# Performance work log

Measured on AMD Instinct MI355X. Metric: run time of the kernel, lower is better.

## Reference

```python
import jax, jax.numpy as jnp
import numpy as np
from jax import lax

T, B, S = 64, 32, 64
V, E, H = 32000, 512, 512

def _p(key, shape, scale=0.05):
    return (jax.random.normal(key, shape, dtype=jnp.float32) * scale)

def setup_inputs() -> dict:
    key = jax.random.key(0)
    ks = jax.random.split(key, 24)
    inp = {
        'trg': jax.random.randint(ks[0], (T, B), 0, V),
        'encoded_src': jax.random.normal(ks[1], (S, B, 2 * H), dtype=jnp.float32),
        'emb': _p(ks[2], (V, E)),
        # LSTM layer 0: input = E + 2H
        'W_ih0': _p(ks[3], (4 * H, E + 2 * H)), 'W_hh0': _p(ks[4], (4 * H, H)),
        'b_ih0': _p(ks[5], (4 * H,)), 'b_hh0': _p(ks[6], (4 * H,)),
        # LSTM layer 1: input = H
        'W_ih1': _p(ks[7], (4 * H, H)), 'W_hh1': _p(ks[8], (4 * H, H)),
        'b_ih1': _p(ks[9], (4 * H,)), 'b_hh1': _p(ks[10], (4 * H,)),
        # attn_annot: 2H -> H
        'Wa': _p(ks[11], (H, 2 * H)), 'ba': _p(ks[12], (H,)),
        # attn_hidden: H -> H
        'Wh': _p(ks[13], (H, H)), 'bh': _p(ks[14], (H,)),
        # other: H -> 1
        'Wo': _p(ks[15], (1, H)), 'bo': _p(ks[16], (1,)),
        # penult: 3H -> E
        'Wp': _p(ks[17], (E, 3 * H)), 'bp': _p(ks[18], (E,)),
        # out bias (weight tied to emb)
        'b_out': _p(ks[19], (V,)),
    }
    return inp

def _lstm_cell(x, h, c, W_ih, W_hh, b_ih, b_hh):
    # PyTorch gate order: i, f, g, o
    g = x @ W_ih.T + b_ih + h @ W_hh.T + b_hh
    i, f, gg, o = jnp.split(g, 4, axis=-1)
    c_new = jax.nn.sigmoid(f) * c + jax.nn.sigmoid(i) * jnp.tanh(gg)
    h_new = jax.nn.sigmoid(o) * jnp.tanh(c_new)
    return h_new, c_new

def reference(trg, encoded_src, emb, W_ih0, W_hh0, b_ih0, b_hh0,
              W_ih1, W_hh1, b_ih1, b_hh1, Wa, ba, Wh, bh, Wo, bo,
              Wp, bp, b_out):
    trg_emb = emb[trg]                                # [T,B,E]
    annot_scores = encoded_src @ Wa.T + ba            # [S,B,H]
    Hd = W_hh0.shape[1]
    Bd = encoded_src.shape[1]
    h0 = jnp.zeros((2, Bd, Hd), dtype=encoded_src.dtype)
    c0 = jnp.zeros((2, Bd, Hd), dtype=encoded_src.dtype)
    ctx0 = jnp.zeros((Bd, encoded_src.shape[2]), dtype=encoded_src.dtype)

    def step(carry, emb_t):
        h, c, ctx = carry
        x = jnp.concatenate([emb_t, ctx], axis=1)      # [B, E+2H]
        h0n, c0n = _lstm_cell(x,   h[0], c[0], W_ih0, W_hh0, b_ih0, b_hh0)
        h1n, c1n = _lstm_cell(h0n, h[1], c[1], W_ih1, W_hh1, b_ih1, b_hh1)
        out = h1n                                      # [B,H]
        hs = out @ Wh.T + bh                           # [B,H]
        e = jnp.tanh(hs[None] + annot_scores) @ Wo.T + bo   # [S,B,1]
        a = jax.nn.softmax(e, axis=0)[..., 0]          # [S,B]
        ctx_new = jnp.einsum('sb,sbd->bd', a, encoded_src)  # [B,2H]
        stacked = jnp.concatenate([out, ctx_new], axis=1)   # [B,3H]
        return (jnp.stack([h0n, h1n]), jnp.stack([c0n, c1n]), ctx_new), stacked

    (h, c, _), all_scores = lax.scan(step, (h0, c0, ctx0), trg_emb)  # all_scores [T,B,3H]
    pen = all_scores @ Wp.T + bp                       # [T,B,E]
    logits = pen @ emb.T + b_out                       # [T,B,V] (tied weights)
    scores = jax.nn.log_softmax(logits, axis=2)
    return (scores, h, c)
```

## Files before the change

### kernel.cpp

```cpp
#include <hip/hip_runtime.h>


typedef unsigned short u16;
typedef short bf16x8 __attribute__((ext_vector_type(8)));
typedef float f32x4 __attribute__((ext_vector_type(4)));

#define MFMA_BF16(a, b, c) __builtin_amdgcn_mfma_f32_16x16x32_bf16((a), (b), (c), 0, 0, 0)

struct __attribute__((aligned(8))) U16x4 { u16 x, y, z, w; };

__device__ __forceinline__ float b2f(u16 u) {
  unsigned v = ((unsigned)u) << 16; float f; __builtin_memcpy(&f, &v, 4); return f;
}
__device__ __forceinline__ u16 f2b(float f) {
  unsigned u; __builtin_memcpy(&u, &f, 4);
  u = (u + 0x7FFFu + ((u >> 16) & 1u)) >> 16;
  return (u16)u;
}
__device__ __forceinline__ float sigm(float x) { return 1.f / (1.f + __expf(-x)); }
__device__ __forceinline__ float tanh_fast(float x) {
  x = fminf(fmaxf(x, -15.f), 15.f);
  float e = __expf(2.f * x);
  return (e - 1.f) / (e + 1.f);
}

__device__ __forceinline__ bf16x8 bl16(const u16* p) {
  bf16x8 v;
  asm volatile("global_load_dwordx4 %0, %1, off sc0 sc1" : "=v"(v) : "v"(p) : "memory");
  return v;
}
__device__ __forceinline__ float blf(const float* p) {
  float v;
  asm volatile("global_load_dword %0, %1, off sc0 sc1" : "=v"(v) : "v"(p) : "memory");
  return v;
}
__device__ __forceinline__ u16 blu16(const u16* p) {
  unsigned v;
  asm volatile("global_load_ushort %0, %1, off sc0 sc1" : "=v"(v) : "v"(p) : "memory");
  return (u16)v;
}
__device__ __forceinline__ void bs16(u16* p, u16 d) {
  unsigned dd = d;
  asm volatile("global_store_short %0, %1, off sc0 sc1" :: "v"(p), "v"(dd) : "memory");
}
__device__ __forceinline__ void bs32u(u16* p, unsigned d) {
  asm volatile("global_store_dword %0, %1, off sc0 sc1" :: "v"(p), "v"(d) : "memory");
}
__device__ __forceinline__ void bsf32(float* p, float d) {
  asm volatile("global_store_dword %0, %1, off sc0 sc1" :: "v"(p), "v"(d) : "memory");
}
__device__ __forceinline__ bf16x8 cl16(const u16* p) {
  bf16x8 v;
  asm volatile("global_load_dwordx4 %0, %1, off" : "=v"(v) : "v"(p));
  return v;
}
__device__ __forceinline__ void vmwait() {
  asm volatile("s_waitcnt vmcnt(0)" ::: "memory");
  __builtin_amdgcn_sched_barrier(0);
}

__global__ void f2b4_kernel(const float* __restrict__ src, u16* __restrict__ dst, long n4) {
  long i = (long)blockIdx.x * blockDim.x + threadIdx.x;
  long stride = (long)gridDim.x * blockDim.x;
  for (; i < n4; i += stride) {
    float4 v = ((const float4*)src)[i];
    U16x4 o; o.x = f2b(v.x); o.y = f2b(v.y); o.z = f2b(v.z); o.w = f2b(v.w);
    ((U16x4*)dst)[i] = o;
  }
}

__global__ void f2b4_strided(const float* __restrict__ src, u16* __restrict__ dst,
                             int rows, int cols4, int sld, int soff, int dld, int doff) {
  int total = rows * cols4;
  for (int i = blockIdx.x * blockDim.x + threadIdx.x; i < total; i += gridDim.x * blockDim.x) {
    int r = i / cols4, c4 = i - r * cols4;
    float4 v = *(const float4*)(src + (size_t)r * sld + soff + c4 * 4);
    U16x4 o; o.x = f2b(v.x); o.y = f2b(v.y); o.z = f2b(v.z); o.w = f2b(v.w);
    *(U16x4*)(dst + (size_t)r * dld + doff + c4 * 4) = o;
  }
}

__global__ void gather_emb_kernel(const int* __restrict__ trg, const float* __restrict__ emb,
                                  u16* __restrict__ out) {
  int r = blockIdx.x;
  int v = trg[r];
  const float* srow = emb + (size_t)v * 512;
  u16* drow = out + (size_t)r * 512;
  for (int e = threadIdx.x; e < 128; e += blockDim.x) {
    float4 x = ((const float4*)srow)[e];
    U16x4 o; o.x = f2b(x.x); o.y = f2b(x.y); o.z = f2b(x.z); o.w = f2b(x.w);
    ((U16x4*)drow)[e] = o;
  }
}

__global__ void annot_tr_kernel(const float* __restrict__ annot, u16* __restrict__ abt) {
  int b = blockIdx.x >> 6, s = blockIdx.x & 63;
  const float* src = annot + (size_t)(s * 32 + b) * 512;
  u16* dst = abt + (size_t)(b * 64 + s) * 512;
  int j = threadIdx.x;
  float4 v = ((const float4*)src)[j];
  U16x4 o; o.x = f2b(v.x); o.y = f2b(v.y); o.z = f2b(v.z); o.w = f2b(v.w);
  ((U16x4*)dst)[j] = o;
}

__global__ void enc_tr_kernel(const float* __restrict__ enc, u16* __restrict__ ebt) {
  int b = blockIdx.x >> 6, s = blockIdx.x & 63;
  const float* src = enc + (size_t)(s * 32 + b) * 1024;
  u16* dst = ebt + (size_t)(b * 64 + s) * 1024;
  int j = threadIdx.x;
  float4 v = ((const float4*)src)[j];
  U16x4 o; o.x = f2b(v.x); o.y = f2b(v.y); o.z = f2b(v.z); o.w = f2b(v.w);
  ((U16x4*)dst)[j] = o;
}

template <int MODE>
__global__ __launch_bounds__(256) void gemm_bt(
    const u16* __restrict__ A, const u16* __restrict__ B,
    float* __restrict__ outF, u16* __restrict__ outB,
    const float* __restrict__ bias0, const float* __restrict__ bias1,
    int N, int K) {
  const int l = threadIdx.x & 63, wv = threadIdx.x >> 6;
  const int m0 = blockIdx.x * 128 + wv * 32;
  const int n0 = blockIdx.y * 64;
  const int kg = ((l >> 4) << 3);
  const u16* Ap0 = A + (size_t)(m0 + (l & 15)) * K + kg;
  const u16* Ap1 = Ap0 + (size_t)16 * K;
  const u16* Bp = B + (size_t)(n0 + (l & 15)) * K + kg;
  f32x4 acc[2][4] = {};
  for (int k0 = 0; k0 < K; k0 += 32) {
    bf16x8 a0 = *(const bf16x8*)(Ap0 + k0);
    bf16x8 a1 = *(const bf16x8*)(Ap1 + k0);
#pragma unroll
    for (int nf = 0; nf < 4; ++nf) {
      bf16x8 bb = *(const bf16x8*)(Bp + (size_t)(nf * 16) * K + k0);
      acc[0][nf] = MFMA_BF16(a0, bb, acc[0][nf]);
      acc[1][nf] = MFMA_BF16(a1, bb, acc[1][nf]);
    }
  }
  float biasv[4];
#pragma unroll
  for (int nf = 0; nf < 4; ++nf) {
    int col = n0 + nf * 16 + (l & 15);
    float bv = bias0 ? bias0[col] : 0.f;
    if (bias1) bv += bias1[col];
    biasv[nf] = bv;
  }
#pragma unroll
  for (int mi = 0; mi < 2; ++mi)
#pragma unroll
    for (int i = 0; i < 4; ++i) {
      int row = m0 + mi * 16 + ((l >> 4) << 2) + i;
#pragma unroll
      for (int nf = 0; nf < 4; ++nf) {
        int col = n0 + nf * 16 + (l & 15);
        float v = acc[mi][nf][i] + biasv[nf];
        if constexpr (MODE == 1)
          outB[(size_t)row * N + col] = f2b(v);
        else
          outF[(size_t)row * N + col] = v;
      }
    }
}

__global__ __launch_bounds__(256) void logits_kernel(
    const u16* __restrict__ A,
    const u16* __restrict__ B,
    const float* __restrict__ bias,
    float* __restrict__ out,
    float* __restrict__ pmax, float* __restrict__ psum) {
  __shared__ float smf[128 * 132];
  const int id = blockIdx.x;
  const int lin = (id & 7) * 500 + (id >> 3);
  const int mt = lin & 15, nt = lin >> 4;
  const int gm = mt * 128, n0 = nt * 128;
  const int l = threadIdx.x & 63, wv = threadIdx.x >> 6;
  const int kg = ((l >> 4) << 3);
  const int m0 = gm + wv * 32;

  const u16* Ap0 = A + (size_t)(m0 + (l & 15)) * 512 + kg;
  const u16* Ap1 = Ap0 + (size_t)16 * 512;
  const u16* Bp = B + (size_t)(n0 + (l & 15)) * 512 + kg;
  f32x4 acc[2][8] = {};
  for (int k0 = 0; k0 < 512; k0 += 32) {
    bf16x8 a0 = *(const bf16x8*)(Ap0 + k0);
    bf16x8 a1 = *(const bf16x8*)(Ap1 + k0);
#pragma unroll
    for (int nf = 0; nf < 8; ++nf) {
      bf16x8 bb = *(const bf16x8*)(Bp + (size_t)(nf * 16) * 512 + k0);
      acc[0][nf] = MFMA_BF16(a0, bb, acc[0][nf]);
      acc[1][nf] = MFMA_BF16(a1, bb, acc[1][nf]);
    }
  }
  float bv[8];
#pragma unroll
  for (int nf = 0; nf < 8; ++nf) bv[nf] = bias[n0 + nf * 16 + (l & 15)];

  float lm[2][4], se[2][4];
#pragma unroll
  for (int mi = 0; mi < 2; ++mi)
#pragma unroll
    for (int i = 0; i < 4; ++i) {
      int rl = wv * 32 + mi * 16 + ((l >> 4) << 2) + i;
      float m_ = -3.4e38f;
#pragma unroll
      for (int nf = 0; nf < 8; ++nf) {
        float v = acc[mi][nf][i] + bv[nf];
        acc[mi][nf][i] = v;
        smf[rl * 132 + nf * 16 + (l & 15)] = v;
        m_ = fmaxf(m_, v);
      }
      lm[mi][i] = m_;
    }
#pragma unroll
  for (int d = 1; d < 16; d <<= 1)
#pragma unroll
    for (int mi = 0; mi < 2; ++mi)
#pragma unroll
      for (int i = 0; i < 4; ++i) lm[mi][i] = fmaxf(lm[mi][i], __shfl_xor(lm[mi][i], d));
#pragma unroll
  for (int mi = 0; mi < 2; ++mi)
#pragma unroll
    for (int i = 0; i < 4; ++i) {
      float s_ = 0.f;
#pragma unroll
      for (int nf = 0; nf < 8; ++nf) s_ += __expf(acc[mi][nf][i] - lm[mi][i]);
      se[mi][i] = s_;
    }
#pragma unroll
  for (int d = 1; d < 16; d <<= 1)
#pragma unroll
    for (int mi = 0; mi < 2; ++mi)
#pragma unroll
      for (int i = 0; i < 4; ++i) se[mi][i] += __shfl_xor(se[mi][i], d);
  if ((l & 15) == 0) {
#pragma unroll
    for (int mi = 0; mi < 2; ++mi)
#pragma unroll
      for (int i = 0; i < 4; ++i) {
        int row = m0 + mi * 16 + ((l >> 4) << 2) + i;
        pmax[(size_t)row * 250 + nt] = lm[mi][i];
        psum[(size_t)row * 250 + nt] = se[mi][i];
      }
  }
  __syncthreads();
#pragma unroll
  for (int r = 0; r < 128; r += 8) {
    int row = r + (threadIdx.x >> 5);
    int c4 = threadIdx.x & 31;
    float4 v = *(float4*)&smf[row * 132 + c4 * 4];
    *(float4*)&out[(size_t)(gm + row) * 32000 + n0 + c4 * 4] = v;
  }
}

__device__ __forceinline__ void grid_barrier(unsigned* flags, unsigned phase) {
  __syncthreads();
  if (threadIdx.x == 0) {
    __hip_atomic_store(flags + blockIdx.x * 32, phase, __ATOMIC_RELAXED,
                       __HIP_MEMORY_SCOPE_AGENT);
  }
  if (threadIdx.x < 32) {
    int spins = 0;
    while (__hip_atomic_load(flags + threadIdx.x * 32, __ATOMIC_RELAXED,
                             __HIP_MEMORY_SCOPE_AGENT) < phase &&
           spins < 2000000) ++spins;
  }
  __syncthreads();
}

__global__ __launch_bounds__(512, 2) void scan_kernel(
    const u16* __restrict__ xW0,
    const u16* __restrict__ Wcat0,
    const u16* __restrict__ Wcat1,
    const u16* __restrict__ Whb,
    const float* __restrict__ b_ih1, const float* __restrict__ b_hh1,
    const float* __restrict__ bh, const float* __restrict__ Wo, const float* __restrict__ bo,
    const u16* __restrict__ annot_bt,
    const u16* __restrict__ enc_bt,
    u16* __restrict__ ctxb,
    u16* __restrict__ h0b,
    u16* __restrict__ h1b,
    float* __restrict__ c0, float* __restrict__ c1,
    float* __restrict__ hs,
    u16* __restrict__ scoresb,
    float* __restrict__ dout_hc,
    unsigned* __restrict__ flags) {
  __shared__ float sm[16384];
  const int w = blockIdx.x;
  const int tid = threadIdx.x;
  const int l = tid & 63, wv = tid >> 6;
  const int jh0 = w * 16;
  const int bE = tid >> 4, jlE = tid & 15;
  unsigned phase = 0;

  float gb1[4];
#pragma unroll
  for (int g = 0; g < 4; ++g) gb1[g] = b_ih1[g * 512 + jh0 + jlE] + b_hh1[g * 512 + jh0 + jlE];
  const float bhv = bh[jh0 + jlE];
  const float bov = bo[0];

  for (int t = 0; t < 64; ++t) {
    const int pA = t & 1;
    {
      const int kg = ((l >> 4) << 3);
      u16 xw[4];
      {
        const u16* xp = xW0 + (size_t)(t * 32 + bE) * 2048 + jh0 + jlE;
#pragma unroll
        for (int g = 0; g < 4; ++g) xw[g] = blu16(xp + g * 512);
      }
      bf16x8 a0[6], a1[6];
#pragma unroll
      for (int kk = 0; kk < 6; ++kk) {
        const int k0 = wv * 192 + kk * 32;
        const u16* ab; int ld, off;
        if (k0 < 1024) { ab = ctxb; ld = 1024; off = k0; }
        else { ab = h0b + pA * 16384; ld = 512; off = k0 - 1024; }
        a0[kk] = bl16(ab + (size_t)(l & 15) * ld + off + kg);
        a1[kk] = bl16(ab + (size_t)((l & 15) + 16) * ld + off + kg);
      }
      vmwait();
      f32x4 acc[2][4] = {};
#pragma unroll
      for (int kk = 0; kk < 6; ++kk) {
        const int k0 = wv * 192 + kk * 32;
#pragma unroll
        for (int g = 0; g < 4; ++g) {
          bf16x8 bb = *(const bf16x8*)(Wcat0 + (size_t)(g * 512 + jh0 + (l & 15)) * 1536 + k0 + kg);
          acc[0][g] = MFMA_BF16(a0[kk], bb, acc[0][g]);
          acc[1][g] = MFMA_BF16(a1[kk], bb, acc[1][g]);
        }
      }
#pragma unroll
      for (int mi = 0; mi < 2; ++mi)
#pragma unroll
        for (int g = 0; g < 4; ++g)
#pragma unroll
          for (int i = 0; i < 4; ++i) {
            int m = mi * 16 + ((l >> 4) << 2) + i;
            sm[(wv * 32 + m) * 64 + g * 16 + (l & 15)] = acc[mi][g][i];
          }
      __syncthreads();
      {
        const int b = bE, jl = jlE, jh = jh0 + jl;
        float gate[4];
#pragma unroll
        for (int g = 0; g < 4; ++g) {
          float s = 0.f;
#pragma unroll
          for (int kv = 0; kv < 8; ++kv) s += sm[(kv * 32 + b) * 64 + g * 16 + jl];
          gate[g] = s + b2f(xw[g]);
        }
        float cn = sigm(gate[1]) * c0[b * 512 + jh] + sigm(gate[0]) * tanh_fast(gate[2]);
        float hn = sigm(gate[3]) * tanh_fast(cn);
        c0[b * 512 + jh] = cn;
        bs16(h0b + (pA ^ 1) * 16384 + b * 512 + jh, f2b(hn));
        if (t == 63) { dout_hc[b * 512 + jh] = hn; dout_hc[32768 + b * 512 + jh] = cn; }
      }
    }
    bf16x8 wB[16];
    {
      ++phase;
      __syncthreads();
      if (tid == 0)
        __hip_atomic_store(flags + blockIdx.x * 32, phase, __ATOMIC_RELAXED,
                           __HIP_MEMORY_SCOPE_AGENT);
      const int kg = ((l >> 4) << 3);
#pragma unroll
      for (int kk = 0; kk < 4; ++kk)
#pragma unroll
        for (int g = 0; g < 4; ++g)
          wB[kk * 4 + g] = cl16(Wcat1 + (size_t)(g * 512 + jh0 + (l & 15)) * 1024 +
                                wv * 128 + kk * 32 + kg);
      if (tid < 32) {
        int spins = 0;
        while (__hip_atomic_load(flags + tid * 32, __ATOMIC_RELAXED,
                                 __HIP_MEMORY_SCOPE_AGENT) < phase &&
               spins < 2000000) ++spins;
      }
      __syncthreads();
    }
    {
      const int kg = ((l >> 4) << 3);
      bf16x8 a0[4], a1[4];
#pragma unroll
      for (int kk = 0; kk < 4; ++kk) {
        const int k0 = wv * 128 + kk * 32;
        const u16* ab; int off;
        if (k0 < 512) { ab = h0b + (pA ^ 1) * 16384; off = k0; }
        else { ab = h1b + pA * 16384; off = k0 - 512; }
        a0[kk] = bl16(ab + (size_t)(l & 15) * 512 + off + kg);
        a1[kk] = bl16(ab + (size_t)((l & 15) + 16) * 512 + off + kg);
      }
      vmwait();
      f32x4 acc[2][4] = {};
#pragma unroll
      for (int kk = 0; kk < 4; ++kk) {
#pragma unroll
        for (int g = 0; g < 4; ++g) {
          acc[0][g] = MFMA_BF16(a0[kk], wB[kk * 4 + g], acc[0][g]);
          acc[1][g] = MFMA_BF16(a1[kk], wB[kk * 4 + g], acc[1][g]);
        }
      }
#pragma unroll
      for (int mi = 0; mi < 2; ++mi)
#pragma unroll
        for (int g = 0; g < 4; ++g)
#pragma unroll
          for (int i = 0; i < 4; ++i) {
            int m = mi * 16 + ((l >> 4) << 2) + i;
            sm[(wv * 32 + m) * 64 + g * 16 + (l & 15)] = acc[mi][g][i];
          }
      __syncthreads();
      {
        const int b = bE, jl = jlE, jh = jh0 + jl;
        float gate[4];
#pragma unroll
        for (int g = 0; g < 4; ++g) {
          float s = 0.f;
#pragma unroll
          for (int kv = 0; kv < 8; ++kv) s += sm[(kv * 32 + b) * 64 + g * 16 + jl];
          gate[g] = s + gb1[g];
        }
        float cn = sigm(gate[1]) * c1[b * 512 + jh] + sigm(gate[0]) * tanh_fast(gate[2]);
        float hn = sigm(gate[3]) * tanh_fast(cn);
        c1[b * 512 + jh] = cn;
        u16 hb = f2b(hn);
        bs16(h1b + (pA ^ 1) * 16384 + b * 512 + jh, hb);
        bs16(scoresb + (size_t)(t * 32 + b) * 1536 + jh, hb);
        if (t == 63) { dout_hc[16384 + b * 512 + jh] = hn; dout_hc[49152 + b * 512 + jh] = cn; }
      }
    }
    bf16x8 wC[2];
    {
      ++phase;
      __syncthreads();
      if (tid == 0)
        __hip_atomic_store(flags + blockIdx.x * 32, phase, __ATOMIC_RELAXED,
                           __HIP_MEMORY_SCOPE_AGENT);
      const int kg = ((l >> 4) << 3);
#pragma unroll
      for (int kk = 0; kk < 2; ++kk)
        wC[kk] = cl16(Whb + (size_t)(jh0 + (l & 15)) * 512 + wv * 64 + kk * 32 + kg);
      if (tid < 32) {
        int spins = 0;
        while (__hip_atomic_load(flags + tid * 32, __ATOMIC_RELAXED,
                                 __HIP_MEMORY_SCOPE_AGENT) < phase &&
               spins < 2000000) ++spins;
      }
      __syncthreads();
    }
    {
      const int kg = ((l >> 4) << 3);
      const u16* h1n = h1b + (pA ^ 1) * 16384;
      bf16x8 a0[2], a1[2];
#pragma unroll
      for (int kk = 0; kk < 2; ++kk) {
        const int k0 = wv * 64 + kk * 32;
        a0[kk] = bl16(h1n + (size_t)(l & 15) * 512 + k0 + kg);
        a1[kk] = bl16(h1n + (size_t)((l & 15) + 16) * 512 + k0 + kg);
      }
      vmwait();
      f32x4 acc2[2] = {};
#pragma unroll
      for (int kk = 0; kk < 2; ++kk) {
        acc2[0] = MFMA_BF16(a0[kk], wC[kk], acc2[0]);
        acc2[1] = MFMA_BF16(a1[kk], wC[kk], acc2[1]);
      }
#pragma unroll
      for (int mi = 0; mi < 2; ++mi)
#pragma unroll
        for (int i = 0; i < 4; ++i)
          sm[(wv * 32 + mi * 16 + ((l >> 4) << 2) + i) * 16 + (l & 15)] = acc2[mi][i];
      __syncthreads();
      {
        const int b = bE, jl = jlE;
        float s = 0.f;
#pragma unroll
        for (int kv = 0; kv < 8; ++kv) s += sm[(kv * 32 + b) * 16 + jl];
        bsf32(hs + b * 512 + jh0 + jl, s + bhv);
      }
    }
    grid_barrier(flags, ++phase);
    {
      const int b = w;
      float* hs_s = sm;
      float* wo_s = sm + 512;
      float* red = sm + 1024;
      float* a_s = sm + 1536;
      float hv = blf(hs + b * 512 + tid);
      float wov = Wo[tid];
      vmwait();
      hs_s[tid] = hv;
      wo_s[tid] = wov;
      __syncthreads();
      const int s_ = tid >> 3, ks = tid & 7;
      const u16* arow = annot_bt + (size_t)(b * 64 + s_) * 512 + ks * 64;
      float accv = 0.f;
#pragma unroll
      for (int kk8 = 0; kk8 < 8; ++kk8) {
        bf16x8 av = *(const bf16x8*)(arow + kk8 * 8);
#pragma unroll
        for (int j = 0; j < 8; ++j) {
          int k = ks * 64 + kk8 * 8 + j;
          accv += tanh_fast(hs_s[k] + b2f((u16)av[j])) * wo_s[k];
        }
      }
      red[tid] = accv;
      __syncthreads();
      if (tid < 64) {
        float e = bov;
#pragma unroll
        for (int j = 0; j < 8; ++j) e += red[tid * 8 + j];
        float mx = e;
#pragma unroll
        for (int d = 1; d < 64; d <<= 1) mx = fmaxf(mx, __shfl_xor(mx, d));
        float p = __expf(e - mx);
        float ss = p;
#pragma unroll
        for (int d = 1; d < 64; d <<= 1) ss += __shfl_xor(ss, d);
        a_s[tid] = p / ss;
      }
      __syncthreads();
      float cx0 = 0.f, cx1 = 0.f;
      const u16* erow = enc_bt + (size_t)b * 65536 + tid * 2;
#pragma unroll 8
      for (int s2 = 0; s2 < 64; ++s2) {
        unsigned ev = *(const unsigned*)(erow + (size_t)s2 * 1024);
        float av = a_s[s2];
        cx0 += av * b2f((u16)(ev & 0xFFFFu));
        cx1 += av * b2f((u16)(ev >> 16));
      }
      unsigned pk = (unsigned)f2b(cx0) | ((unsigned)f2b(cx1) << 16);
      bs32u(ctxb + b * 1024 + tid * 2, pk);
      bs32u(scoresb + (size_t)(t * 32 + b) * 1536 + 512 + tid * 2, pk);
    }
    grid_barrier(flags, ++phase);
  }
}

__global__ __launch_bounds__(256) void lse_kernel(const float* __restrict__ pmax,
                                                  const float* __restrict__ psum,
                                                  float* __restrict__ lse, int nt) {
  __shared__ float red[256];
  const int r = blockIdx.x;
  float m = -3.4e38f;
  for (int j = threadIdx.x; j < nt; j += 256) m = fmaxf(m, pmax[(size_t)r * nt + j]);
  red[threadIdx.x] = m; __syncthreads();
  for (int s = 128; s > 0; s >>= 1) {
    if (threadIdx.x < s) red[threadIdx.x] = fmaxf(red[threadIdx.x], red[threadIdx.x + s]);
    __syncthreads();
  }
  const float M = red[0]; __syncthreads();
  float s_ = 0.f;
  for (int j = threadIdx.x; j < nt; j += 256)
    s_ += psum[(size_t)r * nt + j] * __expf(pmax[(size_t)r * nt + j] - M);
  red[threadIdx.x] = s_; __syncthreads();
  for (int s = 128; s > 0; s >>= 1) {
    if (threadIdx.x < s) red[threadIdx.x] += red[threadIdx.x + s];
    __syncthreads();
  }
  if (threadIdx.x == 0) lse[r] = M + logf(red[0]);
}

__global__ void finalize_kernel(float* __restrict__ out, const float* __restrict__ lse) {
  const long n4 = 16384000;
  for (long i = (long)blockIdx.x * blockDim.x + threadIdx.x; i < n4;
       i += (long)gridDim.x * blockDim.x) {
    float4 v = ((float4*)out)[i];
    float L = lse[i / 8000];
    v.x -= L; v.y -= L; v.z -= L; v.w -= L;
    ((float4*)out)[i] = v;
  }
}

extern "C" void kernel_launch(void* const* d_in, const int* in_sizes, int n_in,
                              void* d_out, int out_size, void* d_ws, size_t ws_size,
                              hipStream_t stream) {
  const int* trg = (const int*)d_in[0];
  const float* enc = (const float*)d_in[1];
  const float* emb = (const float*)d_in[2];
  const float* W_ih0 = (const float*)d_in[3];
  const float* W_hh0 = (const float*)d_in[4];
  const float* b_ih0 = (const float*)d_in[5];
  const float* b_hh0 = (const float*)d_in[6];
  const float* W_ih1 = (const float*)d_in[7];
  const float* W_hh1 = (const float*)d_in[8];
  const float* b_ih1 = (const float*)d_in[9];
  const float* b_hh1 = (const float*)d_in[10];
  const float* Wa = (const float*)d_in[11];
  const float* ba = (const float*)d_in[12];
  const float* Wh = (const float*)d_in[13];
  const float* bh = (const float*)d_in[14];
  const float* Wo = (const float*)d_in[15];
  const float* bo = (const float*)d_in[16];
  const float* Wp = (const float*)d_in[17];
  const float* bp = (const float*)d_in[18];
  const float* b_out = (const float*)d_in[19];
  float* out = (float*)d_out;

  unsigned char* ws = (unsigned char*)d_ws;
  size_t off = 0;
  auto alloc = [&](size_t bytes) -> void* {
    void* p = ws + off; off += (bytes + 255) & ~(size_t)255; return p;
  };
  u16* emb_b = (u16*)alloc(32768000);
  u16* trgemb_b = (u16*)alloc(2097152);
  u16* enc_b = (u16*)alloc(4194304);
  u16* Wemb0_b = (u16*)alloc(2097152);
  u16* Wcat0_b = (u16*)alloc(6291456);
  u16* Wcat1_b = (u16*)alloc(4194304);
  u16* Wa_b = (u16*)alloc(1048576);
  u16* Wh_b = (u16*)alloc(524288);
  u16* Wp_b = (u16*)alloc(1572864);
  u16* xW0_b = (u16*)alloc(8388608);
  float* annot = (float*)alloc(4194304);
  u16* scoresb = (u16*)alloc(6291456);
  u16* pen_b = (u16*)alloc(2097152);
  u16* ctxb = (u16*)alloc(65536);
  u16* h0b = (u16*)alloc(65536);
  u16* h1b = (u16*)alloc(65536);
  float* c0 = (float*)alloc(65536);
  float* c1 = (float*)alloc(65536);
  float* hsbuf = (float*)alloc(65536);
  float* pmax = (float*)alloc(4194304);
  float* psum = (float*)alloc(4194304);
  float* lse = (float*)alloc(8192);
  unsigned* flags = (unsigned*)alloc(4096);
  if (off > ws_size) return;

  u16* annot_bt = (u16*)pmax;
  u16* enc_bt = (u16*)psum;

  hipMemsetAsync(ctxb, 0, 65536, stream);
  hipMemsetAsync(h0b, 0, 65536, stream);
  hipMemsetAsync(h1b, 0, 65536, stream);
  hipMemsetAsync(c0, 0, 65536, stream);
  hipMemsetAsync(c1, 0, 65536, stream);
  hipMemsetAsync(flags, 0, 4096, stream);

  f2b4_kernel<<<1024, 256, 0, stream>>>(emb, emb_b, 4096000);
  f2b4_kernel<<<256, 256, 0, stream>>>(enc, enc_b, 524288);
  f2b4_kernel<<<128, 256, 0, stream>>>(Wa, Wa_b, 131072);
  f2b4_kernel<<<64, 256, 0, stream>>>(Wh, Wh_b, 65536);
  f2b4_kernel<<<128, 256, 0, stream>>>(Wp, Wp_b, 196608);
  f2b4_strided<<<512, 256, 0, stream>>>(W_ih0, Wemb0_b, 2048, 128, 1536, 0, 512, 0);
  f2b4_strided<<<512, 256, 0, stream>>>(W_ih0, Wcat0_b, 2048, 256, 1536, 512, 1536, 0);
  f2b4_strided<<<512, 256, 0, stream>>>(W_hh0, Wcat0_b, 2048, 128, 512, 0, 1536, 1024);
  f2b4_strided<<<512, 256, 0, stream>>>(W_ih1, Wcat1_b, 2048, 128, 512, 0, 1024, 0);
  f2b4_strided<<<512, 256, 0, stream>>>(W_hh1, Wcat1_b, 2048, 128, 512, 0, 1024, 512);
  gather_emb_kernel<<<2048, 128, 0, stream>>>(trg, emb, trgemb_b);
  enc_tr_kernel<<<2048, 256, 0, stream>>>(enc, enc_bt);

  gemm_bt<1><<<dim3(16, 32), 256, 0, stream>>>(trgemb_b, Wemb0_b, nullptr, xW0_b,
                                               b_ih0, b_hh0, 2048, 512);
  gemm_bt<0><<<dim3(16, 8), 256, 0, stream>>>(enc_b, Wa_b, annot, nullptr,
                                              ba, nullptr, 512, 1024);
  annot_tr_kernel<<<2048, 128, 0, stream>>>(annot, annot_bt);

  scan_kernel<<<32, 512, 0, stream>>>(xW0_b, Wcat0_b, Wcat1_b, Wh_b, b_ih1, b_hh1, bh, Wo, bo,
                                      annot_bt, enc_bt, ctxb, h0b, h1b, c0, c1, hsbuf, scoresb,
                                      out + 65536000, flags);
  gemm_bt<1><<<dim3(16, 8), 256, 0, stream>>>(scoresb, Wp_b, nullptr, pen_b,
                                              bp, nullptr, 512, 1536);
  logits_kernel<<<4000, 256, 0, stream>>>(pen_b, emb_b, b_out, out, pmax, psum);
  lse_kernel<<<2048, 256, 0, stream>>>(pmax, psum, lse, 250);
  finalize_kernel<<<2048, 256, 0, stream>>>(out, lse);
}
```

Before: 2.418 ms.

## Replace hs grid-sync with split-K partial products reduced in attention phase

Each block now multiplies its freshly computed 16-column slice of h1 against the matching Wh columns and writes partial hs contributions for all 512 outputs to a global buffer. The attention phase then sums the 32 partials plus bias per batch row. This drops one flag-based all-block barrier per timestep, which removes a synchronization point from the serial scan's critical path. In exchange it adds 2 MB of partial-sum traffic per step and MFMAs that are half zero-padded.

```diff
diff --git a/kernel.cpp b/kernel.cpp
--- a/kernel.cpp
+++ b/kernel.cpp
@@ -280,11 +280,12 @@
     u16* __restrict__ h0b,
     u16* __restrict__ h1b,
     float* __restrict__ c0, float* __restrict__ c1,
-    float* __restrict__ hs,
+    float* __restrict__ ph,
     u16* __restrict__ scoresb,
     float* __restrict__ dout_hc,
     unsigned* __restrict__ flags) {
   __shared__ float sm[16384];
+  __shared__ u16 h1s[512];
   const int w = blockIdx.x;
   const int tid = threadIdx.x;
   const int l = tid & 63, wv = tid >> 6;
@@ -295,7 +296,6 @@
   float gb1[4];
 #pragma unroll
   for (int g = 0; g < 4; ++g) gb1[g] = b_ih1[g * 512 + jh0 + jlE] + b_hh1[g * 512 + jh0 + jlE];
-  const float bhv = bh[jh0 + jlE];
   const float bov = bo[0];
 
   for (int t = 0; t < 64; ++t) {
@@ -427,57 +427,37 @@
         u16 hb = f2b(hn);
         bs16(h1b + (pA ^ 1) * 16384 + b * 512 + jh, hb);
         bs16(scoresb + (size_t)(t * 32 + b) * 1536 + jh, hb);
+        h1s[b * 16 + jl] = hb;
         if (t == 63) { dout_hc[16384 + b * 512 + jh] = hn; dout_hc[49152 + b * 512 + jh] = cn; }
       }
-    }
-    bf16x8 wC[2];
-    {
-      ++phase;
-      __syncthreads();
-      if (tid == 0)
-        __hip_atomic_store(flags + blockIdx.x * 32, phase, __ATOMIC_RELAXED,
-                           __HIP_MEMORY_SCOPE_AGENT);
-      const int kg = ((l >> 4) << 3);
-#pragma unroll
-      for (int kk = 0; kk < 2; ++kk)
-        wC[kk] = cl16(Whb + (size_t)(jh0 + (l & 15)) * 512 + wv * 64 + kk * 32 + kg);
-      if (tid < 32) {
-        int spins = 0;
-        while (__hip_atomic_load(flags + tid * 32, __ATOMIC_RELAXED,
-                                 __HIP_MEMORY_SCOPE_AGENT) < phase &&
-               spins < 2000000) ++spins;
-      }
-      __syncthreads();
-    }
-    {
-      const int kg = ((l >> 4) << 3);
-      const u16* h1n = h1b + (pA ^ 1) * 16384;
-      bf16x8 a0[2], a1[2];
-#pragma unroll
-      for (int kk = 0; kk < 2; ++kk) {
-        const int k0 = wv * 64 + kk * 32;
-        a0[kk] = bl16(h1n + (size_t)(l & 15) * 512 + k0 + kg);
-        a1[kk] = bl16(h1n + (size_t)((l & 15) + 16) * 512 + k0 + kg);
-      }
-      vmwait();
-      f32x4 acc2[2] = {};
-#pragma unroll
-      for (int kk = 0; kk < 2; ++kk) {
-        acc2[0] = MFMA_BF16(a0[kk], wC[kk], acc2[0]);
-        acc2[1] = MFMA_BF16(a1[kk], wC[kk], acc2[1]);
-      }
-#pragma unroll
-      for (int mi = 0; mi < 2; ++mi)
-#pragma unroll
-        for (int i = 0; i < 4; ++i)
-          sm[(wv * 32 + mi * 16 + ((l >> 4) << 2) + i) * 16 + (l & 15)] = acc2[mi][i];
       __syncthreads();
       {
-        const int b = bE, jl = jlE;
-        float s = 0.f;
-#pragma unroll
-        for (int kv = 0; kv < 8; ++kv) s += sm[(kv * 32 + b) * 16 + jl];
-        bsf32(hs + b * 512 + jh0 + jl, s + bhv);
+        const int kk = l >> 4;
+        const int nl = l & 15;
+        const bf16x8 zz = {0, 0, 0, 0, 0, 0, 0, 0};
+        bf16x8 bfr[4];
+#pragma unroll
+        for (int nt = 0; nt < 4; ++nt) {
+          if (kk < 2)
+            bfr[nt] = *(const bf16x8*)(Whb + (size_t)(wv * 64 + nt * 16 + nl) * 512 + jh0 + kk * 8);
+          else
+            bfr[nt] = zz;
+        }
+#pragma unroll
+        for (int mi = 0; mi < 2; ++mi) {
+          bf16x8 af = zz;
+          if (kk < 2) af = *(const bf16x8*)(h1s + (mi * 16 + nl) * 16 + kk * 8);
+#pragma unroll
+          for (int nt = 0; nt < 4; ++nt) {
+            f32x4 pacc = {};
+            pacc = MFMA_BF16(af, bfr[nt], pacc);
+#pragma unroll
+            for (int i = 0; i < 4; ++i) {
+              int b = mi * 16 + kk * 4 + i;
+              bsf32(ph + ((size_t)b * 32 + w) * 512 + wv * 64 + nt * 16 + nl, pacc[i]);
+            }
+          }
+        }
       }
     }
     grid_barrier(flags, ++phase);
@@ -487,11 +467,19 @@
       float* wo_s = sm + 512;
       float* red = sm + 1024;
       float* a_s = sm + 1536;
-      float hv = blf(hs + b * 512 + tid);
-      float wov = Wo[tid];
-      vmwait();
-      hs_s[tid] = hv;
-      wo_s[tid] = wov;
+      {
+        const float* pb = ph + (size_t)b * 32 * 512 + tid;
+        float v[32];
+#pragma unroll
+        for (int ww = 0; ww < 32; ++ww) v[ww] = blf(pb + ww * 512);
+        float accv = bh[tid];
+        float wov = Wo[tid];
+        vmwait();
+#pragma unroll
+        for (int ww = 0; ww < 32; ++ww) accv += v[ww];
+        hs_s[tid] = accv;
+        wo_s[tid] = wov;
+      }
       __syncthreads();
       const int s_ = tid >> 3, ks = tid & 7;
       const u16* arow = annot_bt + (size_t)(b * 64 + s_) * 512 + ks * 64;
@@ -621,7 +609,7 @@
   u16* h1b = (u16*)alloc(65536);
   float* c0 = (float*)alloc(65536);
   float* c1 = (float*)alloc(65536);
-  float* hsbuf = (float*)alloc(65536);
+  float* phs = (float*)alloc(2097152);
   float* pmax = (float*)alloc(4194304);
   float* psum = (float*)alloc(4194304);
   float* lse = (float*)alloc(8192);
@@ -658,7 +646,7 @@
   annot_tr_kernel<<<2048, 128, 0, stream>>>(annot, annot_bt);
 
   scan_kernel<<<32, 512, 0, stream>>>(xW0_b, Wcat0_b, Wcat1_b, Wh_b, b_ih1, b_hh1, bh, Wo, bo,
-                                      annot_bt, enc_bt, ctxb, h0b, h1b, c0, c1, hsbuf, scoresb,
+                                      annot_bt, enc_bt, ctxb, h0b, h1b, c0, c1, phs, scoresb,
                                       out + 65536000, flags);
   gemm_bt<1><<<dim3(16, 8), 256, 0, stream>>>(scoresb, Wp_b, nullptr, pen_b,
                                               bp, nullptr, 512, 1536);
```

New measurement: 4.151 ms. 1.72x slower.
